# Optimization experiments

Hardware: AMD Instinct MI355X
Metric: run time of the kernel (lower is better)

## Reference

```python
import jax, jax.numpy as jnp
import numpy as np

NUM_HEADS = 12
TOP_R = 0.1


def attention_rollout(attn_stack):
    # attn_stack: [L, B, H, N1, N1]; head_fusion='mean'
    A = attn_stack.mean(axis=2)                       # [L, B, N1, N1]
    n1 = A.shape[-1]
    A = A + jnp.eye(n1, dtype=A.dtype)                # residual connection
    A = A / A.sum(axis=-1, keepdims=True)             # row-normalize
    rollout = A[0]
    for l in range(1, A.shape[0]):                    # small fixed loop over layers
        rollout = A[l] @ rollout
    return rollout                                    # [B, N1, N1]


def setup_inputs() -> dict:
    key = jax.random.key(0)
    ks = jax.random.split(key, 7)
    B, N1, D, L, H = 32, 197, 768, 12, NUM_HEADS
    s = 1.0 / np.sqrt(D)
    return {
        "x": jax.random.normal(ks[0], (B, N1, D), dtype=jnp.float32),
        "attn_stack": jax.random.uniform(ks[1], (L, B, H, N1, N1), dtype=jnp.float32),
        "q_w": jax.random.normal(ks[2], (D, D), dtype=jnp.float32) * s,
        "k_w": jax.random.normal(ks[3], (D, D), dtype=jnp.float32) * s,
        "v_w": jax.random.normal(ks[4], (D, D), dtype=jnp.float32) * s,
        "proj_w": jax.random.normal(ks[5], (D, D), dtype=jnp.float32) * s,
        "proj_b": jnp.zeros((D,), dtype=jnp.float32),
    }


def reference(x, attn_stack, q_w, k_w, v_w, proj_w, proj_b):
    B, N1, C = x.shape
    N = N1 - 1
    H = NUM_HEADS
    hd = C // H
    scale = hd ** (-0.5)

    # --- attention rollout (detached in original) -> CLS attention over patches ---
    rollout = attention_rollout(jax.lax.stop_gradient(attn_stack))  # [B, N1, N1]
    cls_attention = rollout[:, 0, 1:]                               # [B, N]
    R = int(N * TOP_R)                                              # static top-R count
    _, top_indices = jax.lax.top_k(cls_attention, R)                # [B, R]

    # --- gather top-R local tokens (shift by 1 to skip CLS) ---
    x_local = jnp.take_along_axis(x, (top_indices + 1)[:, :, None], axis=1)  # [B, R, C]

    # --- projections ---
    q = (x_local @ q_w.T).reshape(B, R, H, hd).transpose(0, 2, 1, 3)   # [B, H, R, hd]
    k = (x @ k_w.T).reshape(B, N1, H, hd).transpose(0, 2, 1, 3)        # [B, H, N1, hd]
    v = (x @ v_w.T).reshape(B, N1, H, hd).transpose(0, 2, 1, 3)        # [B, H, N1, hd]

    # --- cross attention: local queries vs global key/values ---
    attn = jnp.einsum('bhrd,bhnd->bhrn', q, k) * scale                 # [B, H, R, N1]
    attn = jax.nn.softmax(attn, axis=-1)
    out = jnp.einsum('bhrn,bhnd->bhrd', attn, v)                       # [B, H, R, hd]
    out = out.transpose(0, 2, 1, 3).reshape(B, R, C)

    # --- output projection ---
    out = out @ proj_w.T + proj_b
    return out
```

## Files before the change

kernel.cpp:

```cpp
#include <hip/hip_runtime.h>
#include <math.h>

#define L_  12
#define B_  32
#define H_  12
#define N1_ 197
#define D_  768
#define R_  19
#define M_TOK (B_ * N1_)
#define NN (N1_ * N1_)

#define K1_FULL_ROWS  69344
#define K1_ROWS       69376
#define K1_BLOCKS     (K1_ROWS / 4)
#define PACK_ROWS     (M_TOK + 2304)
#define PACK_BLOCKS   ((PACK_ROWS * 12 + 255) / 256)
#define QKV_TILES     630

typedef __attribute__((ext_vector_type(8))) _Float16 f16x8;
typedef __attribute__((ext_vector_type(4))) float f32x4;

__device__ __forceinline__ f32x4 ld4u(const float* p) {
  f32x4 r; __builtin_memcpy(&r, p, 16); return r;
}
__device__ __forceinline__ void st4u(float* p, f32x4 v) {
  __builtin_memcpy(p, &v, 16);
}
__device__ __forceinline__ ushort f2h_bits(float f) {
  _Float16 h = (_Float16)f;
  ushort u; __builtin_memcpy(&u, &h, 2); return u;
}
__device__ __forceinline__ float h2f(ushort u) {
  _Float16 h; __builtin_memcpy(&h, &u, 2); return (float)h;
}

typedef const __attribute__((address_space(1))) void* as1_vp;
typedef __attribute__((address_space(3))) void* as3_vp;
__device__ __forceinline__ void gl_lds16(const void* g, void* s) {
  __builtin_amdgcn_global_load_lds((as1_vp)g, (as3_vp)s, 16, 0, 0);
}

__global__ __launch_bounds__(256) void mega_k1_pack(const float* __restrict__ attn,
                                                    float* __restrict__ P,
                                                    float* __restrict__ dvec,
                                                    const float* __restrict__ x,
                                                    const float* __restrict__ k_w,
                                                    const float* __restrict__ v_w,
                                                    const float* __restrict__ q_w,
                                                    ushort* __restrict__ xpack,
                                                    ushort* __restrict__ wpack) {
  int bid = blockIdx.x;
  if (bid < K1_BLOCKS) {
    int wid = threadIdx.x >> 6;
    int t   = threadIdx.x & 63;
    int row_id = bid * 4 + wid;
    int l, b, i;
    if (row_id < K1_FULL_ROWS) {
      l = row_id / 6304;
      int rem = row_id - l * 6304;
      b = rem / 197;
      i = rem - b * 197;
    } else {
      l = 11; b = row_id - K1_FULL_ROWS; i = 0;
    }
    int lb   = l * B_ + b;
    int prow = lb * N1_ + i;
    const float* base = attn + (size_t)lb * (H_ * NN) + (size_t)i * N1_;
    f32x4 acc = {0.f, 0.f, 0.f, 0.f};
    if (t < 49) {
      const float* p = base + 4 * t;
#pragma unroll
      for (int h = 0; h < H_; ++h) acc += ld4u(p + (size_t)h * NN);
    } else if (t == 49) {
      const float* p = base + 196;
#pragma unroll
      for (int h = 0; h < H_; ++h) acc.x += p[(size_t)h * NN];
    }
    float s = (acc.x + acc.y) + (acc.z + acc.w);
#pragma unroll
    for (int o = 32; o; o >>= 1) s += __shfl_xor(s, o);
    float inv = 1.f / (s + 12.f);
    float* Pr = P + (size_t)prow * N1_;
    if (t < 49)       st4u(Pr + 4 * t, acc * inv);
    else if (t == 49) Pr[196] = acc.x * inv;
    if (t == 0) dvec[prow] = 12.f * inv;
  } else {
    int t = (bid - K1_BLOCKS) * 256 + threadIdx.x;
    if (t >= PACK_ROWS * 12) return;
    int row = t / 12, kb = t - row * 12;
    const float* src;
    ushort* dst;
    if (row < M_TOK) {
      src = x + (size_t)row * D_;
      dst = xpack + (size_t)row * 768;
    } else {
      int wr = row - M_TOK;
      int g = wr / 768, rl = wr - g * 768;
      const float* wsrc = (g == 0) ? k_w : (g == 1) ? v_w : q_w;
      src = wsrc + (size_t)rl * D_;
      dst = wpack + (size_t)wr * 768;
    }
    src += kb * 64;
    dst += kb * 64;
#pragma unroll
    for (int u = 0; u < 8; ++u) {
      float4 f = *(const float4*)(src + u * 8);
      float4 g = *(const float4*)(src + u * 8 + 4);
      f16x8 h;
      h[0] = (_Float16)f.x; h[1] = (_Float16)f.y;
      h[2] = (_Float16)f.z; h[3] = (_Float16)f.w;
      h[4] = (_Float16)g.x; h[5] = (_Float16)g.y;
      h[6] = (_Float16)g.z; h[7] = (_Float16)g.w;
      *(f16x8*)(dst + u * 8) = h;
    }
  }
}

__global__ __launch_bounds__(1024) void k2_chain_topk(const float* __restrict__ P,
                                                      const float* __restrict__ dvec,
                                                      int* __restrict__ gidx) {
  int b = blockIdx.x;
  __shared__ float v[N1_];
  __shared__ float part[4][N1_];
  int t = threadIdx.x, quar = t >> 8, j = t & 255;
  int ibeg = (quar * N1_) / 4;
  bool last50 = (quar == 3);

  if (t < N1_) {
    const float* Pr = P + ((size_t)(11 * B_ + b) * N1_) * N1_;
    v[t] = Pr[t] + (t == 0 ? dvec[(11 * B_ + b) * N1_] : 0.f);
  }

  float cur[50], nxt[50];
  if (j < N1_) {
    const float* Pc = P + ((size_t)(10 * B_ + b) * N1_) * N1_ + j;
#pragma unroll
    for (int u = 0; u < 50; ++u) {
      int i = ibeg + u; if (i > 196) i = 196;
      cur[u] = Pc[(size_t)i * N1_];
    }
  }
  __syncthreads();

  for (int l = 10; l >= 0; --l) {
    if (l > 0 && j < N1_) {
      const float* Pc = P + ((size_t)((l - 1) * B_ + b) * N1_) * N1_ + j;
#pragma unroll
      for (int u = 0; u < 50; ++u) {
        int i = ibeg + u; if (i > 196) i = 196;
        nxt[u] = Pc[(size_t)i * N1_];
      }
    }
    if (j < N1_) {
      float a0 = 0.f, a1 = 0.f, a2 = 0.f, a3 = 0.f;
#pragma unroll
      for (int u = 0; u < 48; u += 4) {
        a0 += v[ibeg + u]     * cur[u];
        a1 += v[ibeg + u + 1] * cur[u + 1];
        a2 += v[ibeg + u + 2] * cur[u + 2];
        a3 += v[ibeg + u + 3] * cur[u + 3];
      }
      a0 += v[ibeg + 48] * cur[48];
      if (last50) a1 += v[ibeg + 49] * cur[49];
      float s = (a0 + a1) + (a2 + a3);
      if (quar == 0) s += v[j] * dvec[(l * B_ + b) * N1_ + j];
      part[quar][j] = s;
    }
    __syncthreads();
    if (t < N1_) v[t] = (part[0][t] + part[1][t]) + (part[2][t] + part[3][t]);
    __syncthreads();
#pragma unroll
    for (int u = 0; u < 50; ++u) cur[u] = nxt[u];
  }

  if (t < 64) {
    float val[4];
    int   idx[4];
#pragma unroll
    for (int c = 0; c < 4; ++c) {
      int n = t + c * 64;
      bool ok = (n < N1_ - 1);
      val[c] = ok ? v[n + 1] : -1e30f;
      idx[c] = ok ? n : (1 << 20);
    }
    for (int r = 0; r < R_; ++r) {
      float bv = val[0];
      int   bi = idx[0];
#pragma unroll
      for (int c = 1; c < 4; ++c)
        if (val[c] > bv || (val[c] == bv && idx[c] < bi)) { bv = val[c]; bi = idx[c]; }
#pragma unroll
      for (int o = 32; o; o >>= 1) {
        float ov = __shfl_xor(bv, o);
        int   oi = __shfl_xor(bi, o);
        if (ov > bv || (ov == bv && oi < bi)) { bv = ov; bi = oi; }
      }
      if (t == 0) gidx[b * R_ + r] = b * N1_ + bi + 1;
#pragma unroll
      for (int c = 0; c < 4; ++c)
        if (idx[c] == bi) val[c] = -1e30f;
    }
  }
}

__global__ __launch_bounds__(256) void gemm_kvq_fast(const ushort* __restrict__ xpack,
                                                     const ushort* __restrict__ wpack,
                                                     const int* __restrict__ gidx,
                                                     ushort* __restrict__ kvb,
                                                     ushort* __restrict__ qbuf) {
  __shared__ __attribute__((aligned(16))) ushort As[128 * 64];
  __shared__ __attribute__((aligned(16))) ushort Bs[128 * 64];
  int tid = threadIdx.x, lane = tid & 63, wid = tid >> 6;
  int wr = wid >> 1, wc = wid & 1;
  int lr = lane & 15, lk = lane >> 4;

  int bid = blockIdx.x;
  int bm, wrow0, ccol0, ldc, Mrows;
  ushort* C;
  bool gath;
  if (bid < 600) {
    bm = bid % 50; int bn = bid / 50;
    wrow0 = bn * 128; ccol0 = bn * 128; ldc = 1536; Mrows = M_TOK;
    C = kvb; gath = false;
  } else {
    int tq = bid - 600;
    bm = tq % 5; int bn = tq / 5;
    wrow0 = 1536 + bn * 128; ccol0 = bn * 128; ldc = 768; Mrows = 608;
    C = qbuf; gath = true;
  }

  const ushort* asrc[4];
  const ushort* bsrc[4];
  ushort* adst[4];
  ushort* bdst[4];
  int lrow = lane >> 3, cpr = lane & 7;
#pragma unroll
  for (int i = 0; i < 4; ++i) {
    int r_loc = wid * 32 + i * 8 + lrow;
    int c     = cpr ^ (r_loc & 7);
    int ga    = bm * 128 + r_loc; if (ga >= Mrows) ga = Mrows - 1;
    int arow  = gath ? gidx[ga] : ga;
    asrc[i] = xpack + (size_t)arow * 768 + c * 8;
    bsrc[i] = wpack + (size_t)(wrow0 + r_loc) * 768 + c * 8;
    adst[i] = &As[(wid * 32 + i * 8) * 64];
    bdst[i] = &Bs[(wid * 32 + i * 8) * 64];
  }

  int o0 = (lk ^ (lr & 7)) * 8;
  int o1 = o0 ^ 32;

  f32x4 acc[4][4] = {};

#pragma unroll
  for (int i = 0; i < 4; ++i) { gl_lds16(asrc[i], adst[i]); gl_lds16(bsrc[i], bdst[i]); }

  for (int kb = 0; kb < 12; ++kb) {
    __syncthreads();
    f16x8 af0[4], af1[4], bf0[4], bf1[4];
#pragma unroll
    for (int m = 0; m < 4; ++m) {
      const ushort* rp = &As[(wr * 64 + m * 16 + lr) * 64];
      af0[m] = *(const f16x8*)(rp + o0);
      af1[m] = *(const f16x8*)(rp + o1);
    }
#pragma unroll
    for (int n = 0; n < 4; ++n) {
      const ushort* rp = &Bs[(wc * 64 + n * 16 + lr) * 64];
      bf0[n] = *(const f16x8*)(rp + o0);
      bf1[n] = *(const f16x8*)(rp + o1);
    }
    __syncthreads();
    if (kb < 11) {
#pragma unroll
      for (int i = 0; i < 4; ++i) {
        gl_lds16(asrc[i] + (kb + 1) * 64, adst[i]);
        gl_lds16(bsrc[i] + (kb + 1) * 64, bdst[i]);
      }
    }
#pragma unroll
    for (int m = 0; m < 4; ++m)
#pragma unroll
      for (int n = 0; n < 4; ++n) {
        acc[m][n] = __builtin_amdgcn_mfma_f32_16x16x32_f16(af0[m], bf0[n], acc[m][n], 0, 0, 0);
        acc[m][n] = __builtin_amdgcn_mfma_f32_16x16x32_f16(af1[m], bf1[n], acc[m][n], 0, 0, 0);
      }
  }

#pragma unroll
  for (int m = 0; m < 4; ++m) {
    int row0 = bm * 128 + wr * 64 + m * 16 + (lane >> 4) * 4;
#pragma unroll
    for (int i = 0; i < 4; ++i) {
      int row = row0 + i;
      if (row < Mrows) {
#pragma unroll
        for (int n = 0; n < 4; ++n) {
          int col = ccol0 + wc * 64 + n * 16 + lr;
          C[(size_t)row * ldc + col] = f2h_bits(acc[m][n][i]);
        }
      }
    }
  }
}

__global__ __launch_bounds__(256) void k5_attn(const ushort* __restrict__ kvb,
                                               const ushort* __restrict__ qb,
                                               float* __restrict__ ctx) {
  int bh = blockIdx.x;
  int b = bh / H_, h = bh % H_;
  __shared__ float ks[N1_][68];
  __shared__ float qs[R_][64];
  __shared__ float sc[R_][200];
  __shared__ float rsum[R_];
  int t = threadIdx.x;
  int lane = t & 63, wid = t >> 6;

  const ushort* kb16 = kvb + (size_t)b * N1_ * 1536 + h * 64;
  for (int n = wid; n < N1_; n += 4)
    ks[n][lane] = h2f(kb16[(size_t)n * 1536 + lane]);
  const ushort* qb16 = qb + (size_t)(b * R_) * 768 + h * 64;
  for (int e = t; e < R_ * 64; e += 256) {
    int r = e >> 6, d = e & 63;
    qs[r][d] = h2f(qb16[(size_t)r * 768 + d]);
  }
  __syncthreads();

  if (t < N1_) {
    float accr[R_];
#pragma unroll
    for (int r = 0; r < R_; ++r) accr[r] = 0.f;
#pragma unroll
    for (int d0 = 0; d0 < 4; ++d0) {
      float4 k0 = *(const float4*)&ks[t][d0 * 16 + 0];
      float4 k1 = *(const float4*)&ks[t][d0 * 16 + 4];
      float4 k2 = *(const float4*)&ks[t][d0 * 16 + 8];
      float4 k3 = *(const float4*)&ks[t][d0 * 16 + 12];
#pragma unroll
      for (int r = 0; r < R_; ++r) {
        float4 q0 = *(const float4*)&qs[r][d0 * 16 + 0];
        float4 q1 = *(const float4*)&qs[r][d0 * 16 + 4];
        float4 q2 = *(const float4*)&qs[r][d0 * 16 + 8];
        float4 q3 = *(const float4*)&qs[r][d0 * 16 + 12];
        accr[r] += k0.x * q0.x + k0.y * q0.y + k0.z * q0.z + k0.w * q0.w
                 + k1.x * q1.x + k1.y * q1.y + k1.z * q1.z + k1.w * q1.w
                 + k2.x * q2.x + k2.y * q2.y + k2.z * q2.z + k2.w * q2.w
                 + k3.x * q3.x + k3.y * q3.y + k3.z * q3.z + k3.w * q3.w;
      }
    }
#pragma unroll
    for (int r = 0; r < R_; ++r) sc[r][t] = accr[r] * 0.125f;
  }
  __syncthreads();

  const ushort* vb16 = kvb + (size_t)b * N1_ * 1536 + 768 + h * 64;
  for (int n = wid; n < N1_; n += 4)
    ks[n][lane] = h2f(vb16[(size_t)n * 1536 + lane]);

  for (int r = wid; r < R_; r += 4) {
    float x0 = sc[r][lane];
    float x1 = sc[r][lane + 64];
    float x2 = sc[r][lane + 128];
    bool ok3 = (lane + 192 < N1_);
    float x3 = ok3 ? sc[r][lane + 192] : -1e30f;
    float m = fmaxf(fmaxf(x0, x1), fmaxf(x2, x3));
#pragma unroll
    for (int o = 32; o; o >>= 1) m = fmaxf(m, __shfl_xor(m, o));
    float e0 = expf(x0 - m), e1 = expf(x1 - m), e2 = expf(x2 - m);
    float e3 = ok3 ? expf(x3 - m) : 0.f;
    float s = e0 + e1 + e2 + e3;
#pragma unroll
    for (int o = 32; o; o >>= 1) s += __shfl_xor(s, o);
    sc[r][lane] = e0; sc[r][lane + 64] = e1; sc[r][lane + 128] = e2;
    if (ok3) sc[r][lane + 192] = e3;
    if (lane == 0) rsum[r] = s;
  }
  __syncthreads();

  int r0 = wid, r1 = wid + 4, r2 = wid + 8, r3 = wid + 12, r4 = wid + 16;
  bool has4 = (r4 < R_);
  float a0 = 0.f, a1 = 0.f, a2 = 0.f, a3 = 0.f, a4 = 0.f;
#pragma unroll 4
  for (int n = 0; n < N1_; ++n) {
    float vv = ks[n][lane];
    a0 += sc[r0][n] * vv;
    a1 += sc[r1][n] * vv;
    a2 += sc[r2][n] * vv;
    a3 += sc[r3][n] * vv;
    if (has4) a4 += sc[r4][n] * vv;
  }
  float* cb = ctx + (size_t)(b * R_) * D_ + h * 64 + lane;
  cb[(size_t)r0 * D_] = a0 / rsum[r0];
  cb[(size_t)r1 * D_] = a1 / rsum[r1];
  cb[(size_t)r2 * D_] = a2 / rsum[r2];
  cb[(size_t)r3 * D_] = a3 / rsum[r3];
  if (has4) cb[(size_t)r4 * D_] = a4 / rsum[r4];
}

#define PK 40
template <int BM, int BN, int MF, int NF>
__global__ __launch_bounds__(256) void gemm_f32in(const float* __restrict__ A,
                                                  const float* __restrict__ W0,
                                                  const float* __restrict__ bias,
                                                  float* __restrict__ C,
                                                  int M, int K, int ldc) {
  __shared__ __attribute__((aligned(16))) ushort As[BM][PK];
  __shared__ __attribute__((aligned(16))) ushort Bs[BN][PK];
  constexpr int TPRA = 256 / BM;
  constexpr int EPTA = 32 / TPRA;
  constexpr int NA4  = EPTA / 4;
  constexpr int TPRB = 256 / BN;
  constexpr int EPTB = 32 / TPRB;
  constexpr int NB4  = EPTB / 4;

  int tid  = threadIdx.x;
  int lane = tid & 63, wid = tid >> 6;
  int wr = wid >> 1, wc = wid & 1;
  int lr = lane & 15, lk = lane >> 4;
  int bm = blockIdx.x, bn = blockIdx.y;

  int arow_s = tid / TPRA;
  int akoff  = (tid % TPRA) * EPTA;
  int ar = bm * BM + arow_s; if (ar >= M) ar = M - 1;
  const float* ap = A + (size_t)ar * K + akoff;

  int brow_s = tid / TPRB;
  int bkoff  = (tid % TPRB) * EPTB;
  int wrow   = bn * BN + brow_s;
  const float* wp = W0 + (size_t)wrow * K + bkoff;

  f32x4 acc[MF][NF] = {};

  float4 pa[NA4], pb[NB4];
#pragma unroll
  for (int u = 0; u < NA4; ++u) pa[u] = *(const float4*)(ap + u * 4);
#pragma unroll
  for (int u = 0; u < NB4; ++u) pb[u] = *(const float4*)(wp + u * 4);

  for (int k0 = 0; k0 < K; k0 += 32) {
#pragma unroll
    for (int u = 0; u < NA4; ++u) {
      ushort4 h;
      h.x = f2h_bits(pa[u].x);
      h.y = f2h_bits(pa[u].y);
      h.z = f2h_bits(pa[u].z);
      h.w = f2h_bits(pa[u].w);
      *(ushort4*)&As[arow_s][akoff + u * 4] = h;
    }
#pragma unroll
    for (int u = 0; u < NB4; ++u) {
      ushort4 h;
      h.x = f2h_bits(pb[u].x);
      h.y = f2h_bits(pb[u].y);
      h.z = f2h_bits(pb[u].z);
      h.w = f2h_bits(pb[u].w);
      *(ushort4*)&Bs[brow_s][bkoff + u * 4] = h;
    }
    __syncthreads();

    int kn = k0 + 32;
    if (kn < K) {
#pragma unroll
      for (int u = 0; u < NA4; ++u) pa[u] = *(const float4*)(ap + kn + u * 4);
#pragma unroll
      for (int u = 0; u < NB4; ++u) pb[u] = *(const float4*)(wp + kn + u * 4);
    }

    f16x8 af[MF], bf[NF];
#pragma unroll
    for (int m = 0; m < MF; ++m)
      af[m] = *(const f16x8*)&As[wr * (BM / 2) + m * 16 + lr][lk * 8];
#pragma unroll
    for (int n = 0; n < NF; ++n)
      bf[n] = *(const f16x8*)&Bs[wc * (BN / 2) + n * 16 + lr][lk * 8];
#pragma unroll
    for (int m = 0; m < MF; ++m)
#pragma unroll
      for (int n = 0; n < NF; ++n)
        acc[m][n] = __builtin_amdgcn_mfma_f32_16x16x32_f16(af[m], bf[n], acc[m][n], 0, 0, 0);
    __syncthreads();
  }

#pragma unroll
  for (int m = 0; m < MF; ++m) {
    int row0 = bm * BM + wr * (BM / 2) + m * 16 + lk * 4;
#pragma unroll
    for (int i = 0; i < 4; ++i) {
      int row = row0 + i;
      if (row < M) {
#pragma unroll
        for (int n = 0; n < NF; ++n) {
          int col = bn * BN + wc * (BN / 2) + n * 16 + lr;
          float vv = acc[m][n][i];
          if (bias) vv += bias[col];
          C[(size_t)row * ldc + col] = vv;
        }
      }
    }
  }
}

extern "C" void kernel_launch(void* const* d_in, const int* in_sizes, int n_in,
                              void* d_out, int out_size, void* d_ws, size_t ws_size,
                              hipStream_t stream) {
  const float* x      = (const float*)d_in[0];
  const float* attn   = (const float*)d_in[1];
  const float* q_w    = (const float*)d_in[2];
  const float* k_w    = (const float*)d_in[3];
  const float* v_w    = (const float*)d_in[4];
  const float* proj_w = (const float*)d_in[5];
  const float* proj_b = (const float*)d_in[6];
  float* out = (float*)d_out;

  char* w = (char*)d_ws;
  auto take = [&](size_t bytes) { char* p = w; w += (bytes + 255) & ~(size_t)255; return p; };
  float*  P     = (float*)take((size_t)L_ * B_ * N1_ * N1_ * 4);
  float*  dvec  = (float*)take((size_t)L_ * B_ * N1_ * 4);
  int*    gidx  = (int*)take(B_ * R_ * 4);
  ushort* kvb   = (ushort*)take((size_t)M_TOK * 1536 * 2);
  ushort* qbuf  = (ushort*)take((size_t)B_ * R_ * D_ * 2);
  float*  ctx   = (float*)take((size_t)B_ * R_ * D_ * 4);
  ushort* xpack = (ushort*)take((size_t)M_TOK * 768 * 2);
  ushort* wpack = (ushort*)take((size_t)2304 * 768 * 2);

  hipLaunchKernelGGL(mega_k1_pack, dim3(K1_BLOCKS + PACK_BLOCKS), dim3(256), 0,
                     stream, attn, P, dvec, x, k_w, v_w, q_w, xpack, wpack);
  hipLaunchKernelGGL(k2_chain_topk, dim3(B_), dim3(1024), 0, stream, P, dvec, gidx);
  hipLaunchKernelGGL(gemm_kvq_fast, dim3(QKV_TILES), dim3(256), 0, stream,
                     xpack, wpack, gidx, kvb, qbuf);
  hipLaunchKernelGGL(k5_attn, dim3(B_ * H_), dim3(256), 0, stream, kvb, qbuf, ctx);
  hipLaunchKernelGGL((gemm_f32in<64, 64, 2, 2>), dim3(10, 12), dim3(256), 0, stream,
                     ctx, proj_w, proj_b, out, B_ * R_, D_, D_);
}
```

Measured before the change: 314.8 us.

## Split head-sum into flat plane streaming and separate row-normalization kernel

```diff
diff --git a/kernel.cpp b/kernel.cpp
--- a/kernel.cpp
+++ b/kernel.cpp
@@ -13,8 +13,16 @@
 #define K1_FULL_ROWS  69344
 #define K1_ROWS       69376
 #define K1_BLOCKS     (K1_ROWS / 4)
+
+#define PLANES_L011   (11 * B_)
+#define CHUNKS_PP     10
+#define F4_PER_PLANE  9703
+#define CHUNK_F4      971
+#define SUMA_BLOCKS   (PLANES_L011 * CHUNKS_PP + B_)
+
 #define PACK_ROWS     (M_TOK + 2304)
 #define PACK_BLOCKS   ((PACK_ROWS * 12 + 255) / 256)
+#define MEGA1_BLOCKS  (SUMA_BLOCKS + PACK_BLOCKS)
 #define QKV_TILES     630
 
 typedef __attribute__((ext_vector_type(8))) _Float16 f16x8;
@@ -40,52 +48,44 @@
   __builtin_amdgcn_global_load_lds((as1_vp)g, (as3_vp)s, 16, 0, 0);
 }
 
-__global__ __launch_bounds__(256) void mega_k1_pack(const float* __restrict__ attn,
-                                                    float* __restrict__ P,
-                                                    float* __restrict__ dvec,
-                                                    const float* __restrict__ x,
-                                                    const float* __restrict__ k_w,
-                                                    const float* __restrict__ v_w,
-                                                    const float* __restrict__ q_w,
-                                                    ushort* __restrict__ xpack,
-                                                    ushort* __restrict__ wpack) {
+__global__ __launch_bounds__(256) void mega_sum_pack(const float* __restrict__ attn,
+                                                     float* __restrict__ P,
+                                                     const float* __restrict__ x,
+                                                     const float* __restrict__ k_w,
+                                                     const float* __restrict__ v_w,
+                                                     const float* __restrict__ q_w,
+                                                     ushort* __restrict__ xpack,
+                                                     ushort* __restrict__ wpack) {
   int bid = blockIdx.x;
-  if (bid < K1_BLOCKS) {
-    int wid = threadIdx.x >> 6;
-    int t   = threadIdx.x & 63;
-    int row_id = bid * 4 + wid;
-    int l, b, i;
-    if (row_id < K1_FULL_ROWS) {
-      l = row_id / 6304;
-      int rem = row_id - l * 6304;
-      b = rem / 197;
-      i = rem - b * 197;
+  if (bid < SUMA_BLOCKS) {
+    int plane, f0, f1;
+    if (bid < PLANES_L011 * CHUNKS_PP) {
+      plane = bid / CHUNKS_PP;
+      int chunk = bid - plane * CHUNKS_PP;
+      f0 = chunk * CHUNK_F4;
+      f1 = f0 + CHUNK_F4; if (f1 > F4_PER_PLANE) f1 = F4_PER_PLANE;
     } else {
-      l = 11; b = row_id - K1_FULL_ROWS; i = 0;
-    }
-    int lb   = l * B_ + b;
-    int prow = lb * N1_ + i;
-    const float* base = attn + (size_t)lb * (H_ * NN) + (size_t)i * N1_;
-    f32x4 acc = {0.f, 0.f, 0.f, 0.f};
-    if (t < 49) {
-      const float* p = base + 4 * t;
-#pragma unroll
-      for (int h = 0; h < H_; ++h) acc += ld4u(p + (size_t)h * NN);
-    } else if (t == 49) {
-      const float* p = base + 196;
-#pragma unroll
-      for (int h = 0; h < H_; ++h) acc.x += p[(size_t)h * NN];
-    }
-    float s = (acc.x + acc.y) + (acc.z + acc.w);
-#pragma unroll
-    for (int o = 32; o; o >>= 1) s += __shfl_xor(s, o);
-    float inv = 1.f / (s + 12.f);
-    float* Pr = P + (size_t)prow * N1_;
-    if (t < 49)       st4u(Pr + 4 * t, acc * inv);
-    else if (t == 49) Pr[196] = acc.x * inv;
-    if (t == 0) dvec[prow] = 12.f * inv;
+      plane = PLANES_L011 + (bid - PLANES_L011 * CHUNKS_PP);
+      f0 = 0; f1 = 50;
+    }
+    const float* base = attn + (size_t)plane * (H_ * NN);
+    float* Pb = P + (size_t)plane * NN;
+    for (int f = f0 + (int)threadIdx.x; f < f1; f += 256) {
+      int fl = f * 4;
+      if (fl + 4 <= NN) {
+        f32x4 a = {0.f, 0.f, 0.f, 0.f};
+#pragma unroll
+        for (int h = 0; h < H_; ++h) a += ld4u(base + (size_t)h * NN + fl);
+        st4u(Pb + fl, a);
+      } else {
+        float a = 0.f;
+#pragma unroll
+        for (int h = 0; h < H_; ++h) a += base[(size_t)h * NN + fl];
+        Pb[fl] = a;
+      }
+    }
   } else {
-    int t = (bid - K1_BLOCKS) * 256 + threadIdx.x;
+    int t = (bid - SUMA_BLOCKS) * 256 + threadIdx.x;
     if (t >= PACK_ROWS * 12) return;
     int row = t / 12, kb = t - row * 12;
     const float* src;
@@ -116,11 +116,40 @@
   }
 }
 
+__global__ __launch_bounds__(256) void rowinv(const float* __restrict__ P,
+                                              float* __restrict__ Inv) {
+  int wid = threadIdx.x >> 6;
+  int t   = threadIdx.x & 63;
+  int row_id = blockIdx.x * 4 + wid;
+  int l, b, i;
+  if (row_id < K1_FULL_ROWS) {
+    l = row_id / 6304;
+    int rem = row_id - l * 6304;
+    b = rem / 197;
+    i = rem - b * 197;
+  } else {
+    l = 11; b = row_id - K1_FULL_ROWS; i = 0;
+  }
+  int prow = (l * B_ + b) * N1_ + i;
+  const float* Pr = P + (size_t)prow * N1_;
+  float s = 0.f;
+  if (t < 49) {
+    f32x4 v = ld4u(Pr + 4 * t);
+    s = (v.x + v.y) + (v.z + v.w);
+  } else if (t == 49) {
+    s = Pr[196];
+  }
+#pragma unroll
+  for (int o = 32; o; o >>= 1) s += __shfl_xor(s, o);
+  if (t == 0) Inv[prow] = 1.f / (s + 12.f);
+}
+
 __global__ __launch_bounds__(1024) void k2_chain_topk(const float* __restrict__ P,
-                                                      const float* __restrict__ dvec,
+                                                      const float* __restrict__ Inv,
                                                       int* __restrict__ gidx) {
   int b = blockIdx.x;
   __shared__ float v[N1_];
+  __shared__ float wv[N1_];
   __shared__ float part[4][N1_];
   int t = threadIdx.x, quar = t >> 8, j = t & 255;
   int ibeg = (quar * N1_) / 4;
@@ -128,7 +157,8 @@
 
   if (t < N1_) {
     const float* Pr = P + ((size_t)(11 * B_ + b) * N1_) * N1_;
-    v[t] = Pr[t] + (t == 0 ? dvec[(11 * B_ + b) * N1_] : 0.f);
+    float iv0 = Inv[(11 * B_ + b) * N1_];
+    v[t] = Pr[t] * iv0 + (t == 0 ? 12.f * iv0 : 0.f);
   }
 
   float cur[50], nxt[50];
@@ -151,19 +181,21 @@
         nxt[u] = Pc[(size_t)i * N1_];
       }
     }
+    if (t < N1_) wv[t] = v[t] * Inv[(l * B_ + b) * N1_ + t];
+    __syncthreads();
     if (j < N1_) {
       float a0 = 0.f, a1 = 0.f, a2 = 0.f, a3 = 0.f;
 #pragma unroll
       for (int u = 0; u < 48; u += 4) {
-        a0 += v[ibeg + u]     * cur[u];
-        a1 += v[ibeg + u + 1] * cur[u + 1];
-        a2 += v[ibeg + u + 2] * cur[u + 2];
-        a3 += v[ibeg + u + 3] * cur[u + 3];
-      }
-      a0 += v[ibeg + 48] * cur[48];
-      if (last50) a1 += v[ibeg + 49] * cur[49];
+        a0 += wv[ibeg + u]     * cur[u];
+        a1 += wv[ibeg + u + 1] * cur[u + 1];
+        a2 += wv[ibeg + u + 2] * cur[u + 2];
+        a3 += wv[ibeg + u + 3] * cur[u + 3];
+      }
+      a0 += wv[ibeg + 48] * cur[48];
+      if (last50) a1 += wv[ibeg + 49] * cur[49];
       float s = (a0 + a1) + (a2 + a3);
-      if (quar == 0) s += v[j] * dvec[(l * B_ + b) * N1_ + j];
+      if (quar == 0) s += 12.f * wv[j];
       part[quar][j] = s;
     }
     __syncthreads();
@@ -513,8 +545,8 @@
 
   char* w = (char*)d_ws;
   auto take = [&](size_t bytes) { char* p = w; w += (bytes + 255) & ~(size_t)255; return p; };
-  float*  P     = (float*)take((size_t)L_ * B_ * N1_ * N1_ * 4);
-  float*  dvec  = (float*)take((size_t)L_ * B_ * N1_ * 4);
+  float*  P     = (float*)take((size_t)L_ * B_ * NN * 4);
+  float*  Inv   = (float*)take((size_t)L_ * B_ * N1_ * 4);
   int*    gidx  = (int*)take(B_ * R_ * 4);
   ushort* kvb   = (ushort*)take((size_t)M_TOK * 1536 * 2);
   ushort* qbuf  = (ushort*)take((size_t)B_ * R_ * D_ * 2);
@@ -522,9 +554,10 @@
   ushort* xpack = (ushort*)take((size_t)M_TOK * 768 * 2);
   ushort* wpack = (ushort*)take((size_t)2304 * 768 * 2);
 
-  hipLaunchKernelGGL(mega_k1_pack, dim3(K1_BLOCKS + PACK_BLOCKS), dim3(256), 0,
-                     stream, attn, P, dvec, x, k_w, v_w, q_w, xpack, wpack);
-  hipLaunchKernelGGL(k2_chain_topk, dim3(B_), dim3(1024), 0, stream, P, dvec, gidx);
+  hipLaunchKernelGGL(mega_sum_pack, dim3(MEGA1_BLOCKS), dim3(256), 0, stream,
+                     attn, P, x, k_w, v_w, q_w, xpack, wpack);
+  hipLaunchKernelGGL(rowinv, dim3(K1_BLOCKS), dim3(256), 0, stream, P, Inv);
+  hipLaunchKernelGGL(k2_chain_topk, dim3(B_), dim3(1024), 0, stream, P, Inv, gidx);
   hipLaunchKernelGGL(gemm_kvq_fast, dim3(QKV_TILES), dim3(256), 0, stream,
                      xpack, wpack, gidx, kvb, qbuf);
   hipLaunchKernelGGL(k5_attn, dim3(B_ * H_), dim3(256), 0, stream, kvb, qbuf, ctx);
```

Result: slower. 329.5 us (+4.7%).

## Process 16 contiguous rows per block in head-mean kernel via LDS staging

Applied to the files above, without the earlier changes.

```diff
diff --git a/kernel.cpp b/kernel.cpp
--- a/kernel.cpp
+++ b/kernel.cpp
@@ -10,12 +10,14 @@
 #define M_TOK (B_ * N1_)
 #define NN (N1_ * N1_)
 
-#define K1_FULL_ROWS  69344
-#define K1_ROWS       69376
-#define K1_BLOCKS     (K1_ROWS / 4)
-#define PACK_ROWS     (M_TOK + 2304)
-#define PACK_BLOCKS   ((PACK_ROWS * 12 + 255) / 256)
-#define QKV_TILES     630
+#define ROWS_PB     16
+#define SUBS_PLB    13
+#define LB_BLOCKS   (11 * B_ * SUBS_PLB)
+#define K1V3_BLOCKS (LB_BLOCKS + B_)
+#define PACK_ROWS   (M_TOK + 2304)
+#define PACK_BLOCKS ((PACK_ROWS * 12 + 255) / 256)
+#define MEGA1_BLOCKS (K1V3_BLOCKS + PACK_BLOCKS)
+#define QKV_TILES   630
 
 typedef __attribute__((ext_vector_type(8))) _Float16 f16x8;
 typedef __attribute__((ext_vector_type(4))) float f32x4;
@@ -50,42 +52,88 @@
                                                     ushort* __restrict__ xpack,
                                                     ushort* __restrict__ wpack) {
   int bid = blockIdx.x;
-  if (bid < K1_BLOCKS) {
-    int wid = threadIdx.x >> 6;
-    int t   = threadIdx.x & 63;
-    int row_id = bid * 4 + wid;
-    int l, b, i;
-    if (row_id < K1_FULL_ROWS) {
-      l = row_id / 6304;
-      int rem = row_id - l * 6304;
-      b = rem / 197;
-      i = rem - b * 197;
+  if (bid < K1V3_BLOCKS) {
+    __shared__ float ps[ROWS_PB * 200];
+    __shared__ float rinv[ROWS_PB];
+    int l, b, i0, nrows;
+    if (bid < LB_BLOCKS) {
+      int lb  = bid / SUBS_PLB;
+      int sub = bid - lb * SUBS_PLB;
+      l = lb >> 5; b = lb & 31;
+      i0 = sub * ROWS_PB;
+      nrows = (i0 + ROWS_PB <= N1_) ? ROWS_PB : (N1_ - i0);
     } else {
-      l = 11; b = row_id - K1_FULL_ROWS; i = 0;
-    }
-    int lb   = l * B_ + b;
-    int prow = lb * N1_ + i;
-    const float* base = attn + (size_t)lb * (H_ * NN) + (size_t)i * N1_;
-    f32x4 acc = {0.f, 0.f, 0.f, 0.f};
-    if (t < 49) {
-      const float* p = base + 4 * t;
-#pragma unroll
-      for (int h = 0; h < H_; ++h) acc += ld4u(p + (size_t)h * NN);
-    } else if (t == 49) {
-      const float* p = base + 196;
-#pragma unroll
-      for (int h = 0; h < H_; ++h) acc.x += p[(size_t)h * NN];
-    }
-    float s = (acc.x + acc.y) + (acc.z + acc.w);
-#pragma unroll
-    for (int o = 32; o; o >>= 1) s += __shfl_xor(s, o);
-    float inv = 1.f / (s + 12.f);
-    float* Pr = P + (size_t)prow * N1_;
-    if (t < 49)       st4u(Pr + 4 * t, acc * inv);
-    else if (t == 49) Pr[196] = acc.x * inv;
-    if (t == 0) dvec[prow] = 12.f * inv;
+      l = 11; b = bid - LB_BLOCKS; i0 = 0; nrows = 1;
+    }
+    int lbi = l * B_ + b;
+    const float* base = attn + (size_t)lbi * (H_ * NN) + (size_t)i0 * N1_;
+    int W  = nrows * N1_;
+    int t  = threadIdx.x;
+
+    for (int p = t; p * 4 < W; p += 256) {
+      int fl = p * 4;
+      if (fl + 4 <= W) {
+        f32x4 a = {0.f, 0.f, 0.f, 0.f};
+#pragma unroll
+        for (int h = 0; h < H_; ++h) a += ld4u(base + (size_t)h * NN + fl);
+        *(f32x4*)&ps[fl] = a;
+      } else {
+        int rem = W - fl;
+        for (int e = 0; e < rem; ++e) {
+          float a = 0.f;
+#pragma unroll
+          for (int h = 0; h < H_; ++h) a += base[(size_t)h * NN + fl + e];
+          ps[fl + e] = a;
+        }
+      }
+    }
+    __syncthreads();
+
+    int wv = t >> 6, ln = t & 63;
+    for (int r = wv; r < nrows; r += 4) {
+      const float* rp = &ps[r * N1_];
+      float s = 0.f;
+      if (ln < 49) {
+        s = (rp[4 * ln] + rp[4 * ln + 1]) + (rp[4 * ln + 2] + rp[4 * ln + 3]);
+      } else if (ln == 49) {
+        s = rp[196];
+      }
+#pragma unroll
+      for (int o = 32; o; o >>= 1) s += __shfl_xor(s, o);
+      float inv = 1.f / (s + 12.f);
+      if (ln == 0) {
+        rinv[r] = inv;
+        dvec[lbi * N1_ + i0 + r] = 12.f * inv;
+      }
+    }
+    __syncthreads();
+
+    float* Pout = P + ((size_t)lbi * N1_ + i0) * N1_;
+    for (int p = t; p * 4 < W; p += 256) {
+      int fl = p * 4;
+      int r0  = fl / N1_;
+      int rem = fl - r0 * N1_;
+      if (fl + 4 <= W) {
+        f32x4 v = *(const f32x4*)&ps[fl];
+        if (rem <= N1_ - 4) {
+          float iv = rinv[r0];
+          v.x *= iv; v.y *= iv; v.z *= iv; v.w *= iv;
+        } else {
+#pragma unroll
+          for (int e = 0; e < 4; ++e)
+            v[e] *= rinv[(rem + e >= N1_) ? r0 + 1 : r0];
+        }
+        st4u(Pout + fl, v);
+      } else {
+        int rem2 = W - fl;
+        for (int e = 0; e < rem2; ++e) {
+          int rr = (fl + e) / N1_;
+          Pout[fl + e] = ps[fl + e] * rinv[rr];
+        }
+      }
+    }
   } else {
-    int t = (bid - K1_BLOCKS) * 256 + threadIdx.x;
+    int t = (bid - K1V3_BLOCKS) * 256 + threadIdx.x;
     if (t >= PACK_ROWS * 12) return;
     int row = t / 12, kb = t - row * 12;
     const float* src;
@@ -522,8 +570,8 @@
   ushort* xpack = (ushort*)take((size_t)M_TOK * 768 * 2);
   ushort* wpack = (ushort*)take((size_t)2304 * 768 * 2);
 
-  hipLaunchKernelGGL(mega_k1_pack, dim3(K1_BLOCKS + PACK_BLOCKS), dim3(256), 0,
-                     stream, attn, P, dvec, x, k_w, v_w, q_w, xpack, wpack);
+  hipLaunchKernelGGL(mega_k1_pack, dim3(MEGA1_BLOCKS), dim3(256), 0, stream,
+                     attn, P, dvec, x, k_w, v_w, q_w, xpack, wpack);
   hipLaunchKernelGGL(k2_chain_topk, dim3(B_), dim3(1024), 0, stream, P, dvec, gidx);
   hipLaunchKernelGGL(gemm_kvq_fast, dim3(QKV_TILES), dim3(256), 0, stream,
                      xpack, wpack, gidx, kvb, qbuf);
```

Measured after the change: 319.7 us. No clear change (+1.6%).
